# Optimization experiments

Measured on AMD Instinct MI355X. Metric: run time of the kernel, lower is better.

## Reference

```python
import jax, jax.numpy as jnp
import numpy as np

B, S = 16, 8192
D_MODEL = 128          # config.moe_intermediate_size
D_HID = 512            # config.intermediate_size
N_EXPERTS = 8
BEH_DIM = 32           # config.behavior_embedding_dim
N_BEH = 16             # config.num_behavior -> embedding rows = N_BEH + 1


def setup_inputs() -> dict:
    key = jax.random.key(0)
    k1, k2, k3, k4, k5, k6 = jax.random.split(key, 6)
    hidden_states = jax.random.normal(k1, (B, S, D_MODEL), dtype=jnp.float32)
    position_index = jax.random.randint(k2, (B, S), 0, N_EXPERTS, dtype=jnp.int32)
    behavior_index = jax.random.randint(k3, (B, S), 0, N_BEH + 1, dtype=jnp.int32)
    din = D_MODEL + BEH_DIM
    # expert weights: wi maps (D_MODEL+BEH_DIM)->D_HID, wo maps D_HID->D_MODEL (no bias)
    Wi = jax.random.normal(k4, (N_EXPERTS, din, D_HID), dtype=jnp.float32) * (din ** -0.5)
    Wo = jax.random.normal(k5, (N_EXPERTS, D_HID, D_MODEL), dtype=jnp.float32) * (D_HID ** -0.5)
    emb = jax.random.normal(k6, (N_BEH + 1, BEH_DIM), dtype=jnp.float32)
    return {"hidden_states": hidden_states, "position_index": position_index,
            "behavior_index": behavior_index, "Wi": Wi, "Wo": Wo, "emb": emb}


def reference(hidden_states, position_index, behavior_index, Wi, Wo, emb):
    # behavior injection: concat learned behavior embedding onto each token
    x = jnp.concatenate([hidden_states, emb[behavior_index]], axis=-1)  # [B,S,Din]
    out = jnp.zeros_like(hidden_states)
    # sparse expert dispatch: each token routed to exactly one expert by position_index
    # (loop over small fixed expert count; dropout is identity at p=0 / eval)
    for e in range(Wi.shape[0]):
        h = jax.nn.relu(jnp.einsum('bsd,dh->bsh', x, Wi[e]))   # [B,S,H]
        y = jnp.einsum('bsh,hd->bsd', h, Wo[e])                # [B,S,D]
        out = out + jnp.where((position_index == e)[..., None], y, 0.0)
    return out
```

## Files before the change

### kernel.cpp

```cpp
#include <hip/hip_runtime.h>
#include <stdint.h>

typedef short bf16x8 __attribute__((ext_vector_type(8)));
typedef float f32x4 __attribute__((ext_vector_type(4)));
typedef unsigned short ushort_t;
typedef ushort_t ushort8 __attribute__((ext_vector_type(8)));

#define TOKENS 131072
#define DMODEL 128
#define DIN 160
#define DHID 512
#define NEXP 8
#define BEH 32
#define CAP 24576
#define MT 128
#define TILES (CAP / MT)

#define OFF_COUNTS 0
#define OFF_LISTS  1024
#define OFF_WIP    (OFF_LISTS + NEXP*CAP*4)
#define OFF_WOP    (OFF_WIP + 8*32*5*64*8*2)

#define SCATTER_BLOCKS (TOKENS / 256)
#define NWI (8*32*5*64)
#define NWO (8*8*16*64)
#define PACK_BLOCKS ((NWI + NWO + 255) / 256)

#define SUPER_SHORTS 18432
#define WO_BASE 10240

typedef const __attribute__((address_space(1))) uint32_t* gu32p;
typedef __attribute__((address_space(3))) uint32_t* lu32p;

__device__ __forceinline__ ushort_t f2b(float f) {
    union { float f; uint32_t u; } x; x.f = f;
    uint32_t r = x.u + 0x7FFF + ((x.u >> 16) & 1);
    return (ushort_t)(r >> 16);
}

__device__ __forceinline__ uint32_t pk2(float lo, float hi) {
    uint32_t a = __float_as_uint(lo) + 0x8000u;
    uint32_t b = __float_as_uint(hi) + 0x8000u;
    return (a >> 16) | (b & 0xFFFF0000u);
}

__global__ __launch_bounds__(256) void prep_kernel(
    const int* __restrict__ pos, int* __restrict__ counts, int* __restrict__ lists,
    const float* __restrict__ Wi, const float* __restrict__ Wo,
    ushort_t* __restrict__ wiP, ushort_t* __restrict__ woP)
{
    __shared__ int lcnt[NEXP];
    __shared__ int lbase[NEXP];
    int tid = threadIdx.x;
    if (blockIdx.x < SCATTER_BLOCKS) {
        if (tid < NEXP) lcnt[tid] = 0;
        __syncthreads();
        int t = blockIdx.x * 256 + tid;
        int e = pos[t];
        int slot = atomicAdd(&lcnt[e], 1);
        __syncthreads();
        if (tid < NEXP) lbase[tid] = atomicAdd(&counts[tid], lcnt[tid]);
        __syncthreads();
        int p = lbase[e] + slot;
        if (p < CAP) lists[e * CAP + p] = t;
        return;
    }
    int idx = (blockIdx.x - SCATTER_BLOCKS) * 256 + tid;
    if (idx < NWI) {
        int L = idx & 63; int r = idx >> 6;
        int s = r % 5; r /= 5;
        int t1 = r & 31; int e = r >> 5;
        int n = t1 * 16 + (L & 15);
        int kb = s * 32 + ((L >> 4) & 3) * 8;
        ushort8 o;
        #pragma unroll
        for (int j = 0; j < 8; ++j)
            o[j] = f2b(Wi[((size_t)e * DIN + kb + j) * DHID + n]);
        *(ushort8*)(wiP + (size_t)idx * 8) = o;
    } else {
        int i2 = idx - NWI;
        if (i2 >= NWO) return;
        int L = i2 & 63; int r = i2 >> 6;
        int ks = r & 15; r >>= 4;
        int t2 = r & 7; int e = r >> 3;
        int n = t2 * 16 + (L & 15);
        int kb = ks * 32 + ((L >> 4) & 3) * 8;
        ushort8 o;
        #pragma unroll
        for (int j = 0; j < 8; ++j)
            o[j] = f2b(Wo[((size_t)e * DHID + kb + j) * DMODEL + n]);
        *(ushort8*)(woP + (size_t)i2 * 8) = o;
    }
}

__device__ __forceinline__ void stage_super(
    const ushort_t* __restrict__ wiPe, const ushort_t* __restrict__ woPe,
    ushort_t* dstBuf, int ss, int tid)
{
    #pragma unroll
    for (int it = 0; it < 9; ++it) {
        int g = it * 256 + tid;
        const ushort_t* src;
        if (g < 1280) {
            src = wiPe + (size_t)ss * 10240 + (size_t)g * 8;
        } else {
            int g2 = g - 1280;
            int n = g2 >> 7, kl = (g2 >> 6) & 1, row = g2 & 63;
            src = woPe + ((size_t)((n * 16 + 2 * ss + kl) * 64 + row)) * 8;
        }
        __builtin_amdgcn_global_load_lds((gu32p)(const void*)src,
                                         (lu32p)(void*)(dstBuf + g * 8), 16, 0, 0);
    }
}

__device__ __forceinline__ bf16x8 load_x8(const float* __restrict__ hidden,
                                          const float* __restrict__ emb,
                                          int t, int bi, int c0) {
    if (t < 0) return (bf16x8)0;
    const float* src = (c0 < DMODEL) ? (hidden + (size_t)t * DMODEL + c0)
                                     : (emb + (size_t)bi * BEH + (c0 - DMODEL));
    f32x4 p0 = *(const f32x4*)src;
    f32x4 p1 = *(const f32x4*)(src + 4);
    uint32_t d0 = pk2(p0[0], p0[1]), d1 = pk2(p0[2], p0[3]);
    uint32_t d2 = pk2(p1[0], p1[1]), d3 = pk2(p1[2], p1[3]);
    return __builtin_bit_cast(bf16x8, (uint4){d0, d1, d2, d3});
}

__global__ __launch_bounds__(256, 2) void expert_gemm(
    const float* __restrict__ hidden, const int* __restrict__ bindex,
    const int* __restrict__ lists, const int* __restrict__ counts,
    const ushort_t* __restrict__ wiP, const ushort_t* __restrict__ woP,
    const float* __restrict__ emb, float* __restrict__ out)
{
    int e = blockIdx.y;
    int tile = blockIdx.x;
    int count = counts[e]; if (count > CAP) count = CAP;
    int base = tile * MT;
    if (base >= count) return;
    int mvalid = count - base; if (mvalid > MT) mvalid = MT;

    __shared__ ushort_t wbuf[2][SUPER_SHORTS];

    int tid = threadIdx.x;
    int lane = tid & 63;
    int w = tid >> 6;
    int l15 = lane & 15;
    int quad = lane >> 4;

    const int* listE = lists + (size_t)e * CAP + base;
    const ushort_t* wiPe = wiP + (size_t)e * 32 * 5 * 64 * 8;
    const ushort_t* woPe = woP + (size_t)e * 8 * 16 * 64 * 8;

    stage_super(wiPe, woPe, wbuf[0], 0, tid);

    bf16x8 xf[2][5];
    int tok[2], bi[2];
    #pragma unroll
    for (int tt = 0; tt < 2; ++tt) {
        int row = w * 32 + tt * 16 + l15;
        tok[tt] = -1; bi[tt] = 0;
        if (row < mvalid) { tok[tt] = listE[row]; bi[tt] = bindex[tok[tt]]; }
    }
    #pragma unroll
    for (int s = 0; s < 5; ++s) {
        int c0 = s * 32 + quad * 8;
        xf[0][s] = load_x8(hidden, emb, tok[0], bi[0], c0);
        xf[1][s] = load_x8(hidden, emb, tok[1], bi[1], c0);
    }

    int srcA = (quad & 1) * 32 + l15;
    int srcB = srcA + 16;
    int selM1 = quad >> 1;

    f32x4 yacc[2][8] = {};

    #pragma unroll 2
    for (int ss = 0; ss < 8; ++ss) {
        int cur = ss & 1;
        __syncthreads();
        if (ss + 1 < 8)
            stage_super(wiPe, woPe, wbuf[cur ^ 1], ss + 1, tid);

        #pragma unroll
        for (int kl = 0; kl < 2; ++kl) {
            const ushort_t* wiS = wbuf[cur] + kl * 5120;
            const ushort_t* woS = wbuf[cur] + WO_BASE;

            f32x4 hacc[2][2] = {};
            #pragma unroll
            for (int s = 0; s < 5; ++s) {
                bf16x8 a0 = *(const bf16x8*)&wiS[(0 * 5 + s) * 512 + lane * 8];
                bf16x8 a1 = *(const bf16x8*)&wiS[(1 * 5 + s) * 512 + lane * 8];
                #pragma unroll
                for (int tt = 0; tt < 2; ++tt) {
                    hacc[0][tt] = __builtin_amdgcn_mfma_f32_16x16x32_bf16(a0, xf[tt][s], hacc[0][tt], 0, 0, 0);
                    hacc[1][tt] = __builtin_amdgcn_mfma_f32_16x16x32_bf16(a1, xf[tt][s], hacc[1][tt], 0, 0, 0);
                }
            }
            bf16x8 afrag[2];
            #pragma unroll
            for (int tt = 0; tt < 2; ++tt) {
                f32x4 h0 = hacc[0][tt], h1 = hacc[1][tt];
                #pragma unroll
                for (int r = 0; r < 4; ++r) {
                    h0[r] = h0[r] > 0.f ? h0[r] : 0.f;
                    h1[r] = h1[r] > 0.f ? h1[r] : 0.f;
                }
                uint32_t p00 = pk2(h0[0], h0[1]), p01 = pk2(h0[2], h0[3]);
                uint32_t p10 = pk2(h1[0], h1[1]), p11 = pk2(h1[2], h1[3]);
                uint32_t a00 = (uint32_t)__shfl((int)p00, srcA);
                uint32_t a01 = (uint32_t)__shfl((int)p01, srcA);
                uint32_t a02 = (uint32_t)__shfl((int)p00, srcB);
                uint32_t a03 = (uint32_t)__shfl((int)p01, srcB);
                uint32_t a10 = (uint32_t)__shfl((int)p10, srcA);
                uint32_t a11 = (uint32_t)__shfl((int)p11, srcA);
                uint32_t a12 = (uint32_t)__shfl((int)p10, srcB);
                uint32_t a13 = (uint32_t)__shfl((int)p11, srcB);
                uint4 dv = { selM1 ? a10 : a00, selM1 ? a11 : a01,
                             selM1 ? a12 : a02, selM1 ? a13 : a03 };
                afrag[tt] = __builtin_bit_cast(bf16x8, dv);
            }
            #pragma unroll
            for (int n = 0; n < 8; ++n) {
                bf16x8 b = *(const bf16x8*)&woS[((n * 2 + kl) * 64 + lane) * 8];
                yacc[0][n] = __builtin_amdgcn_mfma_f32_16x16x32_bf16(afrag[0], b, yacc[0][n], 0, 0, 0);
                yacc[1][n] = __builtin_amdgcn_mfma_f32_16x16x32_bf16(afrag[1], b, yacc[1][n], 0, 0, 0);
            }
        }
    }

    #pragma unroll
    for (int tt = 0; tt < 2; ++tt)
        #pragma unroll
        for (int r = 0; r < 4; ++r) {
            int row = w * 32 + tt * 16 + quad * 4 + r;
            if (row < mvalid) {
                int t = listE[row];
                float* dst = out + (size_t)t * DMODEL + l15;
                #pragma unroll
                for (int n = 0; n < 8; ++n)
                    dst[n * 16] = yacc[tt][n][r];
            }
        }
}

extern "C" void kernel_launch(void* const* d_in, const int* in_sizes, int n_in,
                              void* d_out, int out_size, void* d_ws, size_t ws_size,
                              hipStream_t stream) {
    const float* hidden = (const float*)d_in[0];
    const int*   pos    = (const int*)d_in[1];
    const int*   beh    = (const int*)d_in[2];
    const float* Wi     = (const float*)d_in[3];
    const float* Wo     = (const float*)d_in[4];
    const float* emb    = (const float*)d_in[5];

    char* ws = (char*)d_ws;
    int* counts   = (int*)(ws + OFF_COUNTS);
    int* lists    = (int*)(ws + OFF_LISTS);
    ushort_t* wiP = (ushort_t*)(ws + OFF_WIP);
    ushort_t* woP = (ushort_t*)(ws + OFF_WOP);

    hipMemsetAsync(counts, 0, NEXP * sizeof(int), stream);
    prep_kernel<<<SCATTER_BLOCKS + PACK_BLOCKS, 256, 0, stream>>>(pos, counts, lists, Wi, Wo, wiP, woP);
    expert_gemm<<<dim3(TILES, NEXP), 256, 0, stream>>>(
        hidden, beh, lists, counts, wiP, woP, emb, (float*)d_out);
}
```

Before: 93.91 us.

## Load Wo fragments directly from global into registers, shrink LDS to Wi only

Wo B-fragments now go straight from global memory (L2) into per-lane registers each super-step instead of being staged through LDS. Only Wi stays in the double-buffered LDS pipeline, which cuts LDS per block from about 72KB to 40KB. Launch bounds are raised to 3 blocks per CU so the smaller LDS footprint can give higher occupancy. The trade-off is more register pressure (8 extra bf16x8 fragments) and direct global-load latency inside the loop, where the second kl reload can stall the MFMA chain.

```diff
diff --git a/kernel.cpp b/kernel.cpp
--- a/kernel.cpp
+++ b/kernel.cpp
@@ -26,8 +26,7 @@
 #define NWO (8*8*16*64)
 #define PACK_BLOCKS ((NWI + NWO + 255) / 256)
 
-#define SUPER_SHORTS 18432
-#define WO_BASE 10240
+#define WI_SUPER_SHORTS 10240
 
 typedef const __attribute__((address_space(1))) uint32_t* gu32p;
 typedef __attribute__((address_space(3))) uint32_t* lu32p;
@@ -93,21 +92,13 @@
     }
 }
 
-__device__ __forceinline__ void stage_super(
-    const ushort_t* __restrict__ wiPe, const ushort_t* __restrict__ woPe,
-    ushort_t* dstBuf, int ss, int tid)
+__device__ __forceinline__ void stage_wi64(
+    const ushort_t* __restrict__ wiPe, ushort_t* dstBuf, int ss, int tid)
 {
     #pragma unroll
-    for (int it = 0; it < 9; ++it) {
+    for (int it = 0; it < 5; ++it) {
         int g = it * 256 + tid;
-        const ushort_t* src;
-        if (g < 1280) {
-            src = wiPe + (size_t)ss * 10240 + (size_t)g * 8;
-        } else {
-            int g2 = g - 1280;
-            int n = g2 >> 7, kl = (g2 >> 6) & 1, row = g2 & 63;
-            src = woPe + ((size_t)((n * 16 + 2 * ss + kl) * 64 + row)) * 8;
-        }
+        const ushort_t* src = wiPe + (size_t)ss * 10240 + (size_t)g * 8;
         __builtin_amdgcn_global_load_lds((gu32p)(const void*)src,
                                          (lu32p)(void*)(dstBuf + g * 8), 16, 0, 0);
     }
@@ -126,7 +117,7 @@
     return __builtin_bit_cast(bf16x8, (uint4){d0, d1, d2, d3});
 }
 
-__global__ __launch_bounds__(256, 2) void expert_gemm(
+__global__ __launch_bounds__(256, 3) void expert_gemm(
     const float* __restrict__ hidden, const int* __restrict__ bindex,
     const int* __restrict__ lists, const int* __restrict__ counts,
     const ushort_t* __restrict__ wiP, const ushort_t* __restrict__ woP,
@@ -139,7 +130,7 @@
     if (base >= count) return;
     int mvalid = count - base; if (mvalid > MT) mvalid = MT;
 
-    __shared__ ushort_t wbuf[2][SUPER_SHORTS];
+    __shared__ ushort_t wbuf[2][WI_SUPER_SHORTS];
 
     int tid = threadIdx.x;
     int lane = tid & 63;
@@ -151,7 +142,7 @@
     const ushort_t* wiPe = wiP + (size_t)e * 32 * 5 * 64 * 8;
     const ushort_t* woPe = woP + (size_t)e * 8 * 16 * 64 * 8;
 
-    stage_super(wiPe, woPe, wbuf[0], 0, tid);
+    stage_wi64(wiPe, wbuf[0], 0, tid);
 
     bf16x8 xf[2][5];
     int tok[2], bi[2];
@@ -178,13 +169,24 @@
     for (int ss = 0; ss < 8; ++ss) {
         int cur = ss & 1;
         __syncthreads();
+
+        int ks0 = 2 * ss;
+        bf16x8 wof[8];
+        #pragma unroll
+        for (int n = 0; n < 8; ++n)
+            wof[n] = *(const bf16x8*)&woPe[((size_t)(n * 16 + ks0) * 64 + lane) * 8];
+
         if (ss + 1 < 8)
-            stage_super(wiPe, woPe, wbuf[cur ^ 1], ss + 1, tid);
+            stage_wi64(wiPe, wbuf[cur ^ 1], ss + 1, tid);
 
         #pragma unroll
         for (int kl = 0; kl < 2; ++kl) {
+            if (kl == 1) {
+                #pragma unroll
+                for (int n = 0; n < 8; ++n)
+                    wof[n] = *(const bf16x8*)&woPe[((size_t)(n * 16 + ks0 + 1) * 64 + lane) * 8];
+            }
             const ushort_t* wiS = wbuf[cur] + kl * 5120;
-            const ushort_t* woS = wbuf[cur] + WO_BASE;
 
             f32x4 hacc[2][2] = {};
             #pragma unroll
@@ -222,9 +224,8 @@
             }
             #pragma unroll
             for (int n = 0; n < 8; ++n) {
-                bf16x8 b = *(const bf16x8*)&woS[((n * 2 + kl) * 64 + lane) * 8];
-                yacc[0][n] = __builtin_amdgcn_mfma_f32_16x16x32_bf16(afrag[0], b, yacc[0][n], 0, 0, 0);
-                yacc[1][n] = __builtin_amdgcn_mfma_f32_16x16x32_bf16(afrag[1], b, yacc[1][n], 0, 0, 0);
+                yacc[0][n] = __builtin_amdgcn_mfma_f32_16x16x32_bf16(afrag[0], wof[n], yacc[0][n], 0, 0, 0);
+                yacc[1][n] = __builtin_amdgcn_mfma_f32_16x16x32_bf16(afrag[1], wof[n], yacc[1][n], 0, 0, 0);
             }
         }
     }
```

After: 110.9 us. +18.1%, slower.
